# Optimization experiments

Measured on AMD Instinct MI355X. Metric: run time of the kernel, lower is better.

Reference implementation:

```python
import jax, jax.numpy as jnp
import numpy as np

N = 100000      # nodes
E = 1600000     # edges (before self loops)
IN_F = 128
OUT_F = 32
HEADS = 4
NEG_SLOPE = 0.2


def setup_inputs() -> dict:
    key = jax.random.key(0)
    k1, k2, k3, k4, k5, k6 = jax.random.split(key, 6)
    x = jax.random.normal(k1, (N, IN_F), dtype=jnp.float32)
    edge_index = jax.random.randint(k2, (2, E), 0, N, dtype=jnp.int64)
    # PyG GATConv params: shared linear W [in, H*F], attention vectors att_src/att_dst [1,H,F], bias [H*F]
    glorot = (6.0 / (IN_F + HEADS * OUT_F)) ** 0.5
    W = jax.random.uniform(k3, (IN_F, HEADS * OUT_F), dtype=jnp.float32, minval=-glorot, maxval=glorot)
    ga = (6.0 / (1 + OUT_F)) ** 0.5
    att_src = jax.random.uniform(k4, (HEADS, OUT_F), dtype=jnp.float32, minval=-ga, maxval=ga)
    att_dst = jax.random.uniform(k5, (HEADS, OUT_F), dtype=jnp.float32, minval=-ga, maxval=ga)
    bias = jnp.zeros((HEADS * OUT_F,), dtype=jnp.float32)
    return {"x": x, "edge_index": edge_index, "W": W, "att_src": att_src, "att_dst": att_dst, "bias": bias}


def reference(x, edge_index, W, att_src, att_dst, bias):
    n = x.shape[0]
    # add self loops (PyG add_self_loops=True)
    loops = jnp.arange(n, dtype=edge_index.dtype)
    src = jnp.concatenate([edge_index[0], loops])  # [E+N] message source j
    dst = jnp.concatenate([edge_index[1], loops])  # [E+N] message target i

    h = (x @ W).reshape(n, HEADS, OUT_F)                 # [N,H,F]
    a_src = jnp.sum(h * att_src[None], axis=-1)          # [N,H]
    a_dst = jnp.sum(h * att_dst[None], axis=-1)          # [N,H]

    e = a_src[src] + a_dst[dst]                          # [E',H]
    e = jax.nn.leaky_relu(e, NEG_SLOPE)
    # per-destination softmax over incoming edges
    m = jax.ops.segment_max(e, dst, num_segments=n)      # [N,H]
    ex = jnp.exp(e - m[dst])
    s = jax.ops.segment_sum(ex, dst, num_segments=n)     # [N,H]
    alpha = ex / (s[dst] + 1e-16)                        # [E',H]

    msg = h[src] * alpha[:, :, None]                     # [E',H,F]
    out = jax.ops.segment_sum(msg, dst, num_segments=n)  # [N,H,F]
    return out.reshape(n, HEADS * OUT_F) + bias
```

## Files before the change

kernel.cpp:

```cpp
#include <hip/hip_runtime.h>


#define NEG_SLOPE 0.2f
#define NB_MAX 256
#define BSHIFT 9
#define CHUNK 4096
#define BCAP 12288
#define CAP 11264
#define SS_STRIDE 11520
#define LOG2E 1.4426950408889634f

typedef __attribute__((ext_vector_type(8))) short short8;
typedef __attribute__((ext_vector_type(4))) float f32x4;
typedef __attribute__((ext_vector_type(2))) float f32x2;

__device__ __forceinline__ unsigned int rne16(unsigned int u) {
  return (u + 0x7fffu + ((u >> 16) & 1u)) >> 16;
}
__device__ __forceinline__ unsigned int f2bf_pack(float a, float b) {
  return (rne16(__float_as_uint(b)) << 16) | (rne16(__float_as_uint(a)) & 0xffffu);
}

__global__ __launch_bounds__(256) void k_prep(
    const float* __restrict__ W, unsigned short* __restrict__ Wt,
    int* __restrict__ bcnt) {
  int tid = threadIdx.x;
  if (blockIdx.x == 64) { bcnt[tid] = 0; return; }
  int idx = blockIdx.x * 256 + tid;
  int k = idx >> 7, col = idx & 127;
  Wt[col * 128 + k] = (unsigned short)rne16(__float_as_uint(W[idx]));
}

__global__ __launch_bounds__(256) void k_binmm(
    const int* __restrict__ ei, int* __restrict__ bcnt,
    unsigned int* __restrict__ binned, int E, int Nn, int nb, int nbBin,
    const float* __restrict__ x, const unsigned short* __restrict__ Wt,
    unsigned int* __restrict__ hb,
    const float* __restrict__ attS, const float* __restrict__ attD,
    float* __restrict__ aS, float* __restrict__ aD) {
  __shared__ unsigned int buf[CHUNK];
  __shared__ unsigned char bkt[CHUNK];
  __shared__ int hist[NB_MAX];
  __shared__ int loc[NB_MAX];
  __shared__ int gbase[NB_MAX];
  int tid = threadIdx.x;

  if ((int)blockIdx.x < nbBin) {
    int e0 = blockIdx.x * CHUNK;
    int n = E - e0; if (n > CHUNK) n = CHUNK;

    hist[tid] = 0;
    __syncthreads();

    int dstv[CHUNK / 256];
    int srcv[CHUNK / 256];
    int rankv[CHUNK / 256];
#pragma unroll
    for (int j = 0; j < CHUNK / 256; ++j) {
      int idx = j * 256 + tid;
      dstv[j] = -1;
      if (idx < n) {
        int d = ei[E + e0 + idx];
        srcv[j] = ei[e0 + idx];
        dstv[j] = d;
        rankv[j] = atomicAdd(&hist[d >> BSHIFT], 1);
      }
    }
    __syncthreads();

    if (tid < 64) {
      int base = tid * 4;
      int v0 = hist[base], v1 = hist[base + 1], v2 = hist[base + 2], v3 = hist[base + 3];
      int s = v0 + v1 + v2 + v3;
      int inc = s;
#pragma unroll
      for (int d = 1; d < 64; d <<= 1) {
        int t = __shfl_up(inc, d, 64);
        if (tid >= d) inc += t;
      }
      int ex = inc - s;
      loc[base] = ex; loc[base + 1] = ex + v0;
      loc[base + 2] = ex + v0 + v1; loc[base + 3] = ex + v0 + v1 + v2;
    }
    __syncthreads();

#pragma unroll
    for (int j = 0; j < CHUNK / 256; ++j) {
      if (dstv[j] >= 0) {
        int b = dstv[j] >> BSHIFT;
        int slot = loc[b] + rankv[j];
        buf[slot] = (unsigned)srcv[j] | ((unsigned)(dstv[j] & 511) << 20);
        bkt[slot] = (unsigned char)b;
      }
    }
    for (int b = tid; b < nb; b += 256)
      if (hist[b] > 0) gbase[b] = atomicAdd(&bcnt[b], hist[b]);
    __syncthreads();

    for (int s = tid; s < n; s += 256) {
      int b = bkt[s];
      binned[(unsigned)b * BCAP + gbase[b] + (s - loc[b])] = buf[s];
    }
    return;
  }

  int gbid = blockIdx.x - nbBin;
  int w = tid >> 6, lane = tid & 63;
  int m = lane & 15, q = lane >> 4;
  int r0 = gbid * 64 + w * 16;
  int rowA = r0 + m; if (rowA >= Nn) rowA = Nn - 1;
  const float* xrow = x + (unsigned)rowA * 128u;

  f32x4 acc[8];
#pragma unroll
  for (int t = 0; t < 8; ++t) acc[t] = (f32x4){0.f, 0.f, 0.f, 0.f};

#pragma unroll
  for (int ks = 0; ks < 4; ++ks) {
    int k0 = ks * 32 + q * 8;
    float4 a0 = *(const float4*)(xrow + k0);
    float4 a1 = *(const float4*)(xrow + k0 + 4);
    unsigned au[4];
    au[0] = f2bf_pack(a0.x, a0.y);
    au[1] = f2bf_pack(a0.z, a0.w);
    au[2] = f2bf_pack(a1.x, a1.y);
    au[3] = f2bf_pack(a1.z, a1.w);
    short8 af = *(short8*)au;
#pragma unroll
    for (int t = 0; t < 8; ++t) {
      short8 bf = *(const short8*)(Wt + (unsigned)(t * 16 + m) * 128u + k0);
      acc[t] = __builtin_amdgcn_mfma_f32_16x16x32_bf16(af, bf, acc[t], 0, 0, 0);
    }
  }

  float sSa[4], sSb[4], sDa[4], sDb[4];
#pragma unroll
  for (int u = 0; u < 4; ++u) {
    sSa[u] = attS[u * 32 + m]; sSb[u] = attS[u * 32 + m + 16];
    sDa[u] = attD[u * 32 + m]; sDb[u] = attD[u * 32 + m + 16];
  }

#pragma unroll
  for (int r = 0; r < 4; ++r) {
    int rowo = r0 + q * 4 + r;
    bool ok = rowo < Nn;
    if (ok) {
#pragma unroll
      for (int u = 0; u < 4; ++u)
        hb[(unsigned)rowo * 64u + u * 16 + m] = f2bf_pack(acc[2 * u][r], acc[2 * u + 1][r]);
    }
#pragma unroll
    for (int u = 0; u < 4; ++u) {
      float pS = acc[2 * u][r] * sSa[u] + acc[2 * u + 1][r] * sSb[u];
      float pD = acc[2 * u][r] * sDa[u] + acc[2 * u + 1][r] * sDb[u];
#pragma unroll
      for (int d = 8; d >= 1; d >>= 1) {
        pS += __shfl_down(pS, d, 16);
        pD += __shfl_down(pD, d, 16);
      }
      if (ok && m == 0) {
        aS[(unsigned)rowo * 4u + u] = pS * LOG2E;
        aD[(unsigned)rowo * 4u + u] = pD * LOG2E;
      }
    }
  }
}

__global__ __launch_bounds__(512) void k_scatter2(
    const unsigned int* __restrict__ binned, const int* __restrict__ bcnt,
    int2* __restrict__ off2, int* __restrict__ ssrc, int Nn) {
  __shared__ int cnt[512];
  __shared__ int obuf[CAP];
  __shared__ int wsum[8];
  int b = blockIdx.x, tid = threadIdx.x;
  int node0 = b << BSHIFT;
  int nnodes = Nn - node0; if (nnodes > 512) nnodes = 512;
  int nE = bcnt[b];
  const unsigned* bp = binned + (unsigned)b * BCAP;

  cnt[tid] = 0;
  __syncthreads();
  for (int i = tid; i < nE; i += 512)
    atomicAdd(&cnt[(bp[i] >> 20) & 511u], 1);
  __syncthreads();

  int v = cnt[tid] + (tid < nnodes ? 1 : 0);
  int lane = tid & 63, w = tid >> 6;
  int inc = v;
#pragma unroll
  for (int d = 1; d < 64; d <<= 1) {
    int t = __shfl_up(inc, d, 64);
    if (lane >= d) inc += t;
  }
  if (lane == 63) wsum[w] = inc;
  __syncthreads();
  int wbase = 0;
  for (int ww = 0; ww < w; ++ww) wbase += wsum[ww];
  int ex = wbase + inc - v;
  __syncthreads();

  int csrBase = b * SS_STRIDE;
  if (tid < nnodes) {
    off2[node0 + tid] = make_int2(csrBase + ex, v);
    obuf[ex] = node0 + tid;
  }
  cnt[tid] = ex + 1;
  __syncthreads();

  for (int i = tid; i < nE; i += 512) {
    unsigned p = bp[i];
    int d = (p >> 20) & 511u;
    int pos = atomicAdd(&cnt[d], 1);
    if (pos < CAP) obuf[pos] = (int)(p & 0xFFFFFu);
  }
  __syncthreads();

  int tot = nE + nnodes;
  for (int i = tid; i < tot; i += 512) ssrc[csrBase + i] = obuf[i];
}

__global__ __launch_bounds__(256) void k_aggregate(
    const unsigned int* __restrict__ hb, const float* __restrict__ aS, const float* __restrict__ aD,
    const int2* __restrict__ off2, const int* __restrict__ ssrc,
    const float* __restrict__ bias, float* __restrict__ out, int Nn) {
  int wave = threadIdx.x >> 6;
  int lane = threadIdx.x & 63;
  int node = blockIdx.x * 4 + wave;
  if (node >= Nn) return;
  int un = __builtin_amdgcn_readfirstlane(node);
  unsigned hd = (unsigned)lane >> 4;
  float ad = aD[(unsigned)un * 4u + hd];
  int2 o = off2[un];
  int p0 = o.x;
  int deg = o.y;
  const int* sp = ssrc + p0;
  int nch = deg >> 2;
  f32x2 acc = {0.f, 0.f};
  float denA = 0.f, denB = 0.f;

  int s0 = 0, s1 = 0, s2 = 0, s3 = 0;
  unsigned v0 = 0, v1 = 0, v2 = 0, v3 = 0;
  float a0 = 0.f, a1 = 0.f, a2 = 0.f, a3 = 0.f;
  if (nch > 0) {
    s0 = sp[0]; s1 = sp[1]; s2 = sp[2]; s3 = sp[3];
    v0 = hb[(unsigned)s0 * 64u + lane]; v1 = hb[(unsigned)s1 * 64u + lane];
    v2 = hb[(unsigned)s2 * 64u + lane]; v3 = hb[(unsigned)s3 * 64u + lane];
    a0 = aS[(unsigned)s0 * 4u + hd]; a1 = aS[(unsigned)s1 * 4u + hd];
    a2 = aS[(unsigned)s2 * 4u + hd]; a3 = aS[(unsigned)s3 * 4u + hd];
    sp += 4;
  }
  for (int c = 0; c < nch; ++c) {
    int t0 = 0, t1 = 0, t2 = 0, t3 = 0;
    unsigned w0 = 0, w1 = 0, w2 = 0, w3 = 0;
    float b0 = 0.f, b1 = 0.f, b2 = 0.f, b3 = 0.f;
    if (c + 1 < nch) {
      t0 = sp[0]; t1 = sp[1]; t2 = sp[2]; t3 = sp[3];
      w0 = hb[(unsigned)t0 * 64u + lane]; w1 = hb[(unsigned)t1 * 64u + lane];
      w2 = hb[(unsigned)t2 * 64u + lane]; w3 = hb[(unsigned)t3 * 64u + lane];
      b0 = aS[(unsigned)t0 * 4u + hd]; b1 = aS[(unsigned)t1 * 4u + hd];
      b2 = aS[(unsigned)t2 * 4u + hd]; b3 = aS[(unsigned)t3 * 4u + hd];
      sp += 4;
    }
    float e0 = a0 + ad, e1 = a1 + ad, e2 = a2 + ad, e3 = a3 + ad;
    e0 = fmaxf(e0, NEG_SLOPE * e0); e1 = fmaxf(e1, NEG_SLOPE * e1);
    e2 = fmaxf(e2, NEG_SLOPE * e2); e3 = fmaxf(e3, NEG_SLOPE * e3);
    float x0 = exp2f(e0), x1 = exp2f(e1), x2 = exp2f(e2), x3 = exp2f(e3);
    denA += x0 + x1; denB += x2 + x3;
    f32x2 h0 = { __uint_as_float(v0 << 16), __uint_as_float(v0 & 0xffff0000u) };
    f32x2 h1 = { __uint_as_float(v1 << 16), __uint_as_float(v1 & 0xffff0000u) };
    f32x2 h2 = { __uint_as_float(v2 << 16), __uint_as_float(v2 & 0xffff0000u) };
    f32x2 h3 = { __uint_as_float(v3 << 16), __uint_as_float(v3 & 0xffff0000u) };
    acc = h0 * x0 + acc;
    acc = h1 * x1 + acc;
    acc = h2 * x2 + acc;
    acc = h3 * x3 + acc;
    s0 = t0; s1 = t1; s2 = t2; s3 = t3;
    v0 = w0; v1 = w1; v2 = w2; v3 = w3;
    a0 = b0; a1 = b1; a2 = b2; a3 = b3;
  }
  for (int p = nch << 2; p < deg; ++p) {
    int src = (ssrc + p0)[p];
    float e = aS[(unsigned)src * 4u + hd] + ad;
    e = fmaxf(e, NEG_SLOPE * e);
    float ex = exp2f(e);
    unsigned v = hb[(unsigned)src * 64u + lane];
    f32x2 hh = { __uint_as_float(v << 16), __uint_as_float(v & 0xffff0000u) };
    acc = hh * ex + acc;
    denA += ex;
  }
  float inv = 1.0f / (denA + denB + 1e-16f);
  unsigned col = hd * 32u + ((unsigned)lane & 15u);
  out[(unsigned)un * 128u + col] = acc.x * inv + bias[col];
  out[(unsigned)un * 128u + col + 16u] = acc.y * inv + bias[col + 16];
}

extern "C" void kernel_launch(void* const* d_in, const int* in_sizes, int n_in,
                              void* d_out, int out_size, void* d_ws, size_t ws_size,
                              hipStream_t stream) {
  const float* x    = (const float*)d_in[0];
  const int*   ei   = (const int*)d_in[1];
  const float* W    = (const float*)d_in[2];
  const float* attS = (const float*)d_in[3];
  const float* attD = (const float*)d_in[4];
  const float* bias = (const float*)d_in[5];
  float* out = (float*)d_out;

  const int Nn = in_sizes[0] / 128;
  const int E  = in_sizes[1] / 2;
  const int nb = (Nn + (1 << BSHIFT) - 1) >> BSHIFT;
  const int nbBin = (E + CHUNK - 1) / CHUNK;
  const int nGemm = (Nn + 63) / 64;

  char* ws = (char*)d_ws;
  size_t o = 0;
  auto take = [&](size_t bytes) { void* p = ws + o; o += (bytes + 255) & ~(size_t)255; return p; };
  int2* off2     = (int2*)take((size_t)(Nn + 1) * 8);
  int* ssrc      = (int*)take((size_t)NB_MAX * SS_STRIDE * 4);
  int* bcnt      = (int*)take((size_t)NB_MAX * 4);
  float* aS      = (float*)take((size_t)Nn * 4 * 4);
  float* aD      = (float*)take((size_t)Nn * 4 * 4);
  unsigned short* Wt = (unsigned short*)take((size_t)128 * 128 * 2);
  unsigned int* hb = (unsigned int*)take((size_t)Nn * 64 * 4);
  unsigned int* binned = (unsigned int*)take((size_t)NB_MAX * BCAP * 4);
  (void)ws_size; (void)o;

  k_prep<<<65, 256, 0, stream>>>(W, Wt, bcnt);
  k_binmm<<<nbBin + nGemm, 256, 0, stream>>>(ei, bcnt, binned, E, Nn, nb, nbBin,
                                             x, Wt, hb, attS, attD, aS, aD);
  k_scatter2<<<nb, 512, 0, stream>>>(binned, bcnt, off2, ssrc, Nn);
  k_aggregate<<<(Nn + 3) / 4, 256, 0, stream>>>(hb, aS, aD, off2, ssrc, bias, out, Nn);
}
```

Measured before the change: 233.4 us.

## Split GEMM across bin and scatter kernels, vectorize scatter and aggregate gathers

The node-feature GEMM is moved into a shared device function. One third of its tiles now run alongside the edge-binning kernel and two thirds alongside the per-bucket CSR scatter kernel, so the dense work overlaps both sparse phases. The binning and GEMM blocks grow to 512 threads, the scatter kernel reads and writes through uint4/int4, and the aggregate kernel now processes four edges per iteration with each lane loading a 16-byte feature slice, then reduces across lane groups with shuffles. This is meant to raise memory-level parallelism and balance the load, at the cost of more shuffles and predicated tail handling.

```diff
diff --git a/kernel.cpp b/kernel.cpp
--- a/kernel.cpp
+++ b/kernel.cpp
@@ -31,7 +31,74 @@
   Wt[col * 128 + k] = (unsigned short)rne16(__float_as_uint(W[idx]));
 }
 
-__global__ __launch_bounds__(256) void k_binmm(
+__device__ __forceinline__ void gemm_tile(
+    int gbid, int tid, int Nn,
+    const float* __restrict__ x, const unsigned short* __restrict__ Wt,
+    unsigned int* __restrict__ hb,
+    const float* __restrict__ attS, const float* __restrict__ attD,
+    float* __restrict__ aS, float* __restrict__ aD) {
+  int w = tid >> 6, lane = tid & 63;
+  int m = lane & 15, q = lane >> 4;
+  int r0 = gbid * 128 + w * 16;
+  int rowA = r0 + m; if (rowA >= Nn) rowA = Nn - 1;
+  const float* xrow = x + (unsigned)rowA * 128u;
+
+  f32x4 acc[8];
+#pragma unroll
+  for (int t = 0; t < 8; ++t) acc[t] = (f32x4){0.f, 0.f, 0.f, 0.f};
+
+#pragma unroll
+  for (int ks = 0; ks < 4; ++ks) {
+    int k0 = ks * 32 + q * 8;
+    float4 a0 = *(const float4*)(xrow + k0);
+    float4 a1 = *(const float4*)(xrow + k0 + 4);
+    unsigned au[4];
+    au[0] = f2bf_pack(a0.x, a0.y);
+    au[1] = f2bf_pack(a0.z, a0.w);
+    au[2] = f2bf_pack(a1.x, a1.y);
+    au[3] = f2bf_pack(a1.z, a1.w);
+    short8 af = *(short8*)au;
+#pragma unroll
+    for (int t = 0; t < 8; ++t) {
+      short8 bf = *(const short8*)(Wt + (unsigned)(t * 16 + m) * 128u + k0);
+      acc[t] = __builtin_amdgcn_mfma_f32_16x16x32_bf16(af, bf, acc[t], 0, 0, 0);
+    }
+  }
+
+  float sSa[4], sSb[4], sDa[4], sDb[4];
+#pragma unroll
+  for (int u = 0; u < 4; ++u) {
+    sSa[u] = attS[u * 32 + m]; sSb[u] = attS[u * 32 + m + 16];
+    sDa[u] = attD[u * 32 + m]; sDb[u] = attD[u * 32 + m + 16];
+  }
+
+#pragma unroll
+  for (int r = 0; r < 4; ++r) {
+    int rowo = r0 + q * 4 + r;
+    bool ok = rowo < Nn;
+    if (ok) {
+#pragma unroll
+      for (int u = 0; u < 4; ++u)
+        hb[(unsigned)rowo * 64u + u * 16 + m] = f2bf_pack(acc[2 * u][r], acc[2 * u + 1][r]);
+    }
+#pragma unroll
+    for (int u = 0; u < 4; ++u) {
+      float pS = acc[2 * u][r] * sSa[u] + acc[2 * u + 1][r] * sSb[u];
+      float pD = acc[2 * u][r] * sDa[u] + acc[2 * u + 1][r] * sDb[u];
+#pragma unroll
+      for (int d = 8; d >= 1; d >>= 1) {
+        pS += __shfl_down(pS, d, 16);
+        pD += __shfl_down(pD, d, 16);
+      }
+      if (ok && m == 0) {
+        aS[(unsigned)rowo * 4u + u] = pS * LOG2E;
+        aD[(unsigned)rowo * 4u + u] = pD * LOG2E;
+      }
+    }
+  }
+}
+
+__global__ __launch_bounds__(512) void k_bin(
     const int* __restrict__ ei, int* __restrict__ bcnt,
     unsigned int* __restrict__ binned, int E, int Nn, int nb, int nbBin,
     const float* __restrict__ x, const unsigned short* __restrict__ Wt,
@@ -45,134 +112,85 @@
   __shared__ int gbase[NB_MAX];
   int tid = threadIdx.x;
 
-  if ((int)blockIdx.x < nbBin) {
-    int e0 = blockIdx.x * CHUNK;
-    int n = E - e0; if (n > CHUNK) n = CHUNK;
-
-    hist[tid] = 0;
-    __syncthreads();
-
-    int dstv[CHUNK / 256];
-    int srcv[CHUNK / 256];
-    int rankv[CHUNK / 256];
-#pragma unroll
-    for (int j = 0; j < CHUNK / 256; ++j) {
-      int idx = j * 256 + tid;
-      dstv[j] = -1;
-      if (idx < n) {
-        int d = ei[E + e0 + idx];
-        srcv[j] = ei[e0 + idx];
-        dstv[j] = d;
-        rankv[j] = atomicAdd(&hist[d >> BSHIFT], 1);
-      }
-    }
-    __syncthreads();
-
-    if (tid < 64) {
-      int base = tid * 4;
-      int v0 = hist[base], v1 = hist[base + 1], v2 = hist[base + 2], v3 = hist[base + 3];
-      int s = v0 + v1 + v2 + v3;
-      int inc = s;
-#pragma unroll
-      for (int d = 1; d < 64; d <<= 1) {
-        int t = __shfl_up(inc, d, 64);
-        if (tid >= d) inc += t;
-      }
-      int ex = inc - s;
-      loc[base] = ex; loc[base + 1] = ex + v0;
-      loc[base + 2] = ex + v0 + v1; loc[base + 3] = ex + v0 + v1 + v2;
-    }
-    __syncthreads();
-
-#pragma unroll
-    for (int j = 0; j < CHUNK / 256; ++j) {
-      if (dstv[j] >= 0) {
-        int b = dstv[j] >> BSHIFT;
-        int slot = loc[b] + rankv[j];
-        buf[slot] = (unsigned)srcv[j] | ((unsigned)(dstv[j] & 511) << 20);
-        bkt[slot] = (unsigned char)b;
-      }
-    }
-    for (int b = tid; b < nb; b += 256)
-      if (hist[b] > 0) gbase[b] = atomicAdd(&bcnt[b], hist[b]);
-    __syncthreads();
-
-    for (int s = tid; s < n; s += 256) {
-      int b = bkt[s];
-      binned[(unsigned)b * BCAP + gbase[b] + (s - loc[b])] = buf[s];
-    }
+  if ((int)blockIdx.x >= nbBin) {
+    gemm_tile(blockIdx.x - nbBin, tid, Nn, x, Wt, hb, attS, attD, aS, aD);
     return;
   }
 
-  int gbid = blockIdx.x - nbBin;
-  int w = tid >> 6, lane = tid & 63;
-  int m = lane & 15, q = lane >> 4;
-  int r0 = gbid * 64 + w * 16;
-  int rowA = r0 + m; if (rowA >= Nn) rowA = Nn - 1;
-  const float* xrow = x + (unsigned)rowA * 128u;
-
-  f32x4 acc[8];
-#pragma unroll
-  for (int t = 0; t < 8; ++t) acc[t] = (f32x4){0.f, 0.f, 0.f, 0.f};
-
-#pragma unroll
-  for (int ks = 0; ks < 4; ++ks) {
-    int k0 = ks * 32 + q * 8;
-    float4 a0 = *(const float4*)(xrow + k0);
-    float4 a1 = *(const float4*)(xrow + k0 + 4);
-    unsigned au[4];
-    au[0] = f2bf_pack(a0.x, a0.y);
-    au[1] = f2bf_pack(a0.z, a0.w);
-    au[2] = f2bf_pack(a1.x, a1.y);
-    au[3] = f2bf_pack(a1.z, a1.w);
-    short8 af = *(short8*)au;
-#pragma unroll
-    for (int t = 0; t < 8; ++t) {
-      short8 bf = *(const short8*)(Wt + (unsigned)(t * 16 + m) * 128u + k0);
-      acc[t] = __builtin_amdgcn_mfma_f32_16x16x32_bf16(af, bf, acc[t], 0, 0, 0);
-    }
-  }
-
-  float sSa[4], sSb[4], sDa[4], sDb[4];
-#pragma unroll
-  for (int u = 0; u < 4; ++u) {
-    sSa[u] = attS[u * 32 + m]; sSb[u] = attS[u * 32 + m + 16];
-    sDa[u] = attD[u * 32 + m]; sDb[u] = attD[u * 32 + m + 16];
-  }
-
-#pragma unroll
-  for (int r = 0; r < 4; ++r) {
-    int rowo = r0 + q * 4 + r;
-    bool ok = rowo < Nn;
-    if (ok) {
-#pragma unroll
-      for (int u = 0; u < 4; ++u)
-        hb[(unsigned)rowo * 64u + u * 16 + m] = f2bf_pack(acc[2 * u][r], acc[2 * u + 1][r]);
-    }
-#pragma unroll
-    for (int u = 0; u < 4; ++u) {
-      float pS = acc[2 * u][r] * sSa[u] + acc[2 * u + 1][r] * sSb[u];
-      float pD = acc[2 * u][r] * sDa[u] + acc[2 * u + 1][r] * sDb[u];
-#pragma unroll
-      for (int d = 8; d >= 1; d >>= 1) {
-        pS += __shfl_down(pS, d, 16);
-        pD += __shfl_down(pD, d, 16);
-      }
-      if (ok && m == 0) {
-        aS[(unsigned)rowo * 4u + u] = pS * LOG2E;
-        aD[(unsigned)rowo * 4u + u] = pD * LOG2E;
-      }
-    }
-  }
-}
-
-__global__ __launch_bounds__(512) void k_scatter2(
+  int e0 = blockIdx.x * CHUNK;
+  int n = E - e0; if (n > CHUNK) n = CHUNK;
+
+  if (tid < NB_MAX) hist[tid] = 0;
+  __syncthreads();
+
+  int dstv[CHUNK / 512];
+  int srcv[CHUNK / 512];
+  int rankv[CHUNK / 512];
+#pragma unroll
+  for (int j = 0; j < CHUNK / 512; ++j) {
+    int idx = j * 512 + tid;
+    dstv[j] = -1;
+    if (idx < n) {
+      int d = ei[E + e0 + idx];
+      srcv[j] = ei[e0 + idx];
+      dstv[j] = d;
+      rankv[j] = atomicAdd(&hist[d >> BSHIFT], 1);
+    }
+  }
+  __syncthreads();
+
+  if (tid < 64) {
+    int base = tid * 4;
+    int v0 = hist[base], v1 = hist[base + 1], v2 = hist[base + 2], v3 = hist[base + 3];
+    int s = v0 + v1 + v2 + v3;
+    int inc = s;
+#pragma unroll
+    for (int d = 1; d < 64; d <<= 1) {
+      int t = __shfl_up(inc, d, 64);
+      if (tid >= d) inc += t;
+    }
+    int ex = inc - s;
+    loc[base] = ex; loc[base + 1] = ex + v0;
+    loc[base + 2] = ex + v0 + v1; loc[base + 3] = ex + v0 + v1 + v2;
+  }
+  __syncthreads();
+
+#pragma unroll
+  for (int j = 0; j < CHUNK / 512; ++j) {
+    if (dstv[j] >= 0) {
+      int b = dstv[j] >> BSHIFT;
+      int slot = loc[b] + rankv[j];
+      buf[slot] = (unsigned)srcv[j] | ((unsigned)(dstv[j] & 511) << 20);
+      bkt[slot] = (unsigned char)b;
+    }
+  }
+  for (int b = tid; b < nb; b += 512)
+    if (hist[b] > 0) gbase[b] = atomicAdd(&bcnt[b], hist[b]);
+  __syncthreads();
+
+  for (int s = tid; s < n; s += 512) {
+    int b = bkt[s];
+    binned[(unsigned)b * BCAP + gbase[b] + (s - loc[b])] = buf[s];
+  }
+}
+
+__global__ __launch_bounds__(512) void k_scatgemm(
     const unsigned int* __restrict__ binned, const int* __restrict__ bcnt,
-    int2* __restrict__ off2, int* __restrict__ ssrc, int Nn) {
+    int2* __restrict__ off2, int* __restrict__ ssrc, int Nn, int nb, int nGemmA,
+    const float* __restrict__ x, const unsigned short* __restrict__ Wt,
+    unsigned int* __restrict__ hb,
+    const float* __restrict__ attS, const float* __restrict__ attD,
+    float* __restrict__ aS, float* __restrict__ aD) {
   __shared__ int cnt[512];
   __shared__ int obuf[CAP];
   __shared__ int wsum[8];
   int b = blockIdx.x, tid = threadIdx.x;
+
+  if (b >= nb) {
+    gemm_tile(nGemmA + (b - nb), tid, Nn, x, Wt, hb, attS, attD, aS, aD);
+    return;
+  }
+
   int node0 = b << BSHIFT;
   int nnodes = Nn - node0; if (nnodes > 512) nnodes = 512;
   int nE = bcnt[b];
@@ -180,7 +198,15 @@
 
   cnt[tid] = 0;
   __syncthreads();
-  for (int i = tid; i < nE; i += 512)
+  int nE4 = nE >> 2;
+  for (int i = tid; i < nE4; i += 512) {
+    uint4 p = *(const uint4*)(bp + 4 * i);
+    atomicAdd(&cnt[(p.x >> 20) & 511u], 1);
+    atomicAdd(&cnt[(p.y >> 20) & 511u], 1);
+    atomicAdd(&cnt[(p.z >> 20) & 511u], 1);
+    atomicAdd(&cnt[(p.w >> 20) & 511u], 1);
+  }
+  for (int i = (nE4 << 2) + tid; i < nE; i += 512)
     atomicAdd(&cnt[(bp[i] >> 20) & 511u], 1);
   __syncthreads();
 
@@ -207,7 +233,14 @@
   cnt[tid] = ex + 1;
   __syncthreads();
 
-  for (int i = tid; i < nE; i += 512) {
+  for (int i = tid; i < nE4; i += 512) {
+    uint4 p = *(const uint4*)(bp + 4 * i);
+    { int d = (p.x >> 20) & 511u; int pos = atomicAdd(&cnt[d], 1); if (pos < CAP) obuf[pos] = (int)(p.x & 0xFFFFFu); }
+    { int d = (p.y >> 20) & 511u; int pos = atomicAdd(&cnt[d], 1); if (pos < CAP) obuf[pos] = (int)(p.y & 0xFFFFFu); }
+    { int d = (p.z >> 20) & 511u; int pos = atomicAdd(&cnt[d], 1); if (pos < CAP) obuf[pos] = (int)(p.z & 0xFFFFFu); }
+    { int d = (p.w >> 20) & 511u; int pos = atomicAdd(&cnt[d], 1); if (pos < CAP) obuf[pos] = (int)(p.w & 0xFFFFFu); }
+  }
+  for (int i = (nE4 << 2) + tid; i < nE; i += 512) {
     unsigned p = bp[i];
     int d = (p >> 20) & 511u;
     int pos = atomicAdd(&cnt[d], 1);
@@ -216,82 +249,89 @@
   __syncthreads();
 
   int tot = nE + nnodes;
-  for (int i = tid; i < tot; i += 512) ssrc[csrBase + i] = obuf[i];
+  int tot4 = tot >> 2;
+  for (int i = tid; i < tot4; i += 512)
+    *(int4*)(ssrc + csrBase + 4 * i) = *(const int4*)(obuf + 4 * i);
+  for (int i = (tot4 << 2) + tid; i < tot; i += 512)
+    ssrc[csrBase + i] = obuf[i];
 }
 
 __global__ __launch_bounds__(256) void k_aggregate(
-    const unsigned int* __restrict__ hb, const float* __restrict__ aS, const float* __restrict__ aD,
-    const int2* __restrict__ off2, const int* __restrict__ ssrc,
-    const float* __restrict__ bias, float* __restrict__ out, int Nn) {
+    const unsigned int* __restrict__ hb, const float* __restrict__ aS,
+    const float* __restrict__ aD, const int2* __restrict__ off2,
+    const int* __restrict__ ssrc, const float* __restrict__ bias,
+    float* __restrict__ out, int Nn) {
   int wave = threadIdx.x >> 6;
   int lane = threadIdx.x & 63;
   int node = blockIdx.x * 4 + wave;
   if (node >= Nn) return;
   int un = __builtin_amdgcn_readfirstlane(node);
-  unsigned hd = (unsigned)lane >> 4;
-  float ad = aD[(unsigned)un * 4u + hd];
+  int q = lane >> 4, k = lane & 15;
+  int u = k >> 2;
+  float ad = aD[(unsigned)un * 4u + u];
   int2 o = off2[un];
-  int p0 = o.x;
-  int deg = o.y;
+  int p0 = o.x, deg = o.y;
   const int* sp = ssrc + p0;
-  int nch = deg >> 2;
-  f32x2 acc = {0.f, 0.f};
-  float denA = 0.f, denB = 0.f;
-
-  int s0 = 0, s1 = 0, s2 = 0, s3 = 0;
-  unsigned v0 = 0, v1 = 0, v2 = 0, v3 = 0;
-  float a0 = 0.f, a1 = 0.f, a2 = 0.f, a3 = 0.f;
-  if (nch > 0) {
-    s0 = sp[0]; s1 = sp[1]; s2 = sp[2]; s3 = sp[3];
-    v0 = hb[(unsigned)s0 * 64u + lane]; v1 = hb[(unsigned)s1 * 64u + lane];
-    v2 = hb[(unsigned)s2 * 64u + lane]; v3 = hb[(unsigned)s3 * 64u + lane];
-    a0 = aS[(unsigned)s0 * 4u + hd]; a1 = aS[(unsigned)s1 * 4u + hd];
-    a2 = aS[(unsigned)s2 * 4u + hd]; a3 = aS[(unsigned)s3 * 4u + hd];
-    sp += 4;
-  }
-  for (int c = 0; c < nch; ++c) {
-    int t0 = 0, t1 = 0, t2 = 0, t3 = 0;
-    unsigned w0 = 0, w1 = 0, w2 = 0, w3 = 0;
-    float b0 = 0.f, b1 = 0.f, b2 = 0.f, b3 = 0.f;
-    if (c + 1 < nch) {
-      t0 = sp[0]; t1 = sp[1]; t2 = sp[2]; t3 = sp[3];
-      w0 = hb[(unsigned)t0 * 64u + lane]; w1 = hb[(unsigned)t1 * 64u + lane];
-      w2 = hb[(unsigned)t2 * 64u + lane]; w3 = hb[(unsigned)t3 * 64u + lane];
-      b0 = aS[(unsigned)t0 * 4u + hd]; b1 = aS[(unsigned)t1 * 4u + hd];
-      b2 = aS[(unsigned)t2 * 4u + hd]; b3 = aS[(unsigned)t3 * 4u + hd];
-      sp += 4;
-    }
-    float e0 = a0 + ad, e1 = a1 + ad, e2 = a2 + ad, e3 = a3 + ad;
-    e0 = fmaxf(e0, NEG_SLOPE * e0); e1 = fmaxf(e1, NEG_SLOPE * e1);
-    e2 = fmaxf(e2, NEG_SLOPE * e2); e3 = fmaxf(e3, NEG_SLOPE * e3);
-    float x0 = exp2f(e0), x1 = exp2f(e1), x2 = exp2f(e2), x3 = exp2f(e3);
-    denA += x0 + x1; denB += x2 + x3;
-    f32x2 h0 = { __uint_as_float(v0 << 16), __uint_as_float(v0 & 0xffff0000u) };
-    f32x2 h1 = { __uint_as_float(v1 << 16), __uint_as_float(v1 & 0xffff0000u) };
-    f32x2 h2 = { __uint_as_float(v2 << 16), __uint_as_float(v2 & 0xffff0000u) };
-    f32x2 h3 = { __uint_as_float(v3 << 16), __uint_as_float(v3 & 0xffff0000u) };
-    acc = h0 * x0 + acc;
-    acc = h1 * x1 + acc;
-    acc = h2 * x2 + acc;
-    acc = h3 * x3 + acc;
-    s0 = t0; s1 = t1; s2 = t2; s3 = t3;
-    v0 = w0; v1 = w1; v2 = w2; v3 = w3;
-    a0 = b0; a1 = b1; a2 = b2; a3 = b3;
-  }
-  for (int p = nch << 2; p < deg; ++p) {
-    int src = (ssrc + p0)[p];
-    float e = aS[(unsigned)src * 4u + hd] + ad;
+  int niter = (deg + 3) >> 2;
+
+  f32x2 ac0 = {0.f, 0.f}, ac1 = {0.f, 0.f}, ac2 = {0.f, 0.f}, ac3 = {0.f, 0.f};
+  float den = 0.f;
+
+  int ei0 = q;
+  int idx0 = ei0 < deg ? ei0 : 0;
+  int s_c = sp[idx0];
+  uint4 v_c = *(const uint4*)(hb + (unsigned)s_c * 64u + 4 * k);
+  float a_c = aS[(unsigned)s_c * 4u + u];
+  bool ok_c = ei0 < deg;
+
+  for (int it = 0; it < niter; ++it) {
+    int s_n = 0; uint4 v_n = {0, 0, 0, 0}; float a_n = 0.f; bool ok_n = false;
+    if (it + 1 < niter) {
+      int ein = (it + 1) * 4 + q;
+      int idx = ein < deg ? ein : 0;
+      s_n = sp[idx];
+      v_n = *(const uint4*)(hb + (unsigned)s_n * 64u + 4 * k);
+      a_n = aS[(unsigned)s_n * 4u + u];
+      ok_n = ein < deg;
+    }
+    float e = a_c + ad;
     e = fmaxf(e, NEG_SLOPE * e);
     float ex = exp2f(e);
-    unsigned v = hb[(unsigned)src * 64u + lane];
-    f32x2 hh = { __uint_as_float(v << 16), __uint_as_float(v & 0xffff0000u) };
-    acc = hh * ex + acc;
-    denA += ex;
-  }
-  float inv = 1.0f / (denA + denB + 1e-16f);
-  unsigned col = hd * 32u + ((unsigned)lane & 15u);
-  out[(unsigned)un * 128u + col] = acc.x * inv + bias[col];
-  out[(unsigned)un * 128u + col + 16u] = acc.y * inv + bias[col + 16];
+    ex = ok_c ? ex : 0.f;
+    den += ex;
+    f32x2 h0 = { __uint_as_float(v_c.x << 16), __uint_as_float(v_c.x & 0xffff0000u) };
+    f32x2 h1 = { __uint_as_float(v_c.y << 16), __uint_as_float(v_c.y & 0xffff0000u) };
+    f32x2 h2 = { __uint_as_float(v_c.z << 16), __uint_as_float(v_c.z & 0xffff0000u) };
+    f32x2 h3 = { __uint_as_float(v_c.w << 16), __uint_as_float(v_c.w & 0xffff0000u) };
+    ac0 = h0 * ex + ac0;
+    ac1 = h1 * ex + ac1;
+    ac2 = h2 * ex + ac2;
+    ac3 = h3 * ex + ac3;
+    s_c = s_n; v_c = v_n; a_c = a_n; ok_c = ok_n;
+  }
+
+  ac0.x += __shfl_xor(ac0.x, 16, 64); ac0.x += __shfl_xor(ac0.x, 32, 64);
+  ac0.y += __shfl_xor(ac0.y, 16, 64); ac0.y += __shfl_xor(ac0.y, 32, 64);
+  ac1.x += __shfl_xor(ac1.x, 16, 64); ac1.x += __shfl_xor(ac1.x, 32, 64);
+  ac1.y += __shfl_xor(ac1.y, 16, 64); ac1.y += __shfl_xor(ac1.y, 32, 64);
+  ac2.x += __shfl_xor(ac2.x, 16, 64); ac2.x += __shfl_xor(ac2.x, 32, 64);
+  ac2.y += __shfl_xor(ac2.y, 16, 64); ac2.y += __shfl_xor(ac2.y, 32, 64);
+  ac3.x += __shfl_xor(ac3.x, 16, 64); ac3.x += __shfl_xor(ac3.x, 32, 64);
+  ac3.y += __shfl_xor(ac3.y, 16, 64); ac3.y += __shfl_xor(ac3.y, 32, 64);
+  den  += __shfl_xor(den, 16, 64);  den  += __shfl_xor(den, 32, 64);
+
+  if (lane < 16) {
+    float inv = 1.0f / (den + 1e-16f);
+    int cb = u * 32 + 4 * (k & 3);
+    float4 blo = *(const float4*)(bias + cb);
+    float4 bhi = *(const float4*)(bias + cb + 16);
+    float4 rlo = { ac0.x * inv + blo.x, ac1.x * inv + blo.y,
+                   ac2.x * inv + blo.z, ac3.x * inv + blo.w };
+    float4 rhi = { ac0.y * inv + bhi.x, ac1.y * inv + bhi.y,
+                   ac2.y * inv + bhi.z, ac3.y * inv + bhi.w };
+    *(float4*)(out + (unsigned)un * 128u + cb) = rlo;
+    *(float4*)(out + (unsigned)un * 128u + cb + 16) = rhi;
+  }
 }
 
 extern "C" void kernel_launch(void* const* d_in, const int* in_sizes, int n_in,
@@ -309,7 +349,9 @@
   const int E  = in_sizes[1] / 2;
   const int nb = (Nn + (1 << BSHIFT) - 1) >> BSHIFT;
   const int nbBin = (E + CHUNK - 1) / CHUNK;
-  const int nGemm = (Nn + 63) / 64;
+  const int nGemm = (Nn + 127) / 128;
+  const int nGemmA = nGemm / 3;
+  const int nGemmB = nGemm - nGemmA;
 
   char* ws = (char*)d_ws;
   size_t o = 0;
@@ -325,8 +367,9 @@
   (void)ws_size; (void)o;
 
   k_prep<<<65, 256, 0, stream>>>(W, Wt, bcnt);
-  k_binmm<<<nbBin + nGemm, 256, 0, stream>>>(ei, bcnt, binned, E, Nn, nb, nbBin,
-                                             x, Wt, hb, attS, attD, aS, aD);
-  k_scatter2<<<nb, 512, 0, stream>>>(binned, bcnt, off2, ssrc, Nn);
+  k_bin<<<nbBin + nGemmA, 512, 0, stream>>>(ei, bcnt, binned, E, Nn, nb, nbBin,
+                                            x, Wt, hb, attS, attD, aS, aD);
+  k_scatgemm<<<nb + nGemmB, 512, 0, stream>>>(binned, bcnt, off2, ssrc, Nn, nb,
+                                              nGemmA, x, Wt, hb, attS, attD, aS, aD);
   k_aggregate<<<(Nn + 3) / 4, 256, 0, stream>>>(hb, aS, aD, off2, ssrc, bias, out, Nn);
 }
```

Measured after the change: 252.0 us. +8.0%, slower.
